# Optimization experiments

Hardware: AMD Instinct MI355X
Metric: run time of the kernel (lower is better)

The kernel has to match this reference:

```python
import jax, jax.numpy as jnp
import numpy as np

B, T, H = 2, 2048, 1024
L = 256          # latent_dim = hidden // compression_ratio
F = 2048         # intermediate_size = hidden * mlp_ratio
E = 7            # routed experts = num_experts - num_shared
K = 2            # top_k
BASE, SCALE_ROPE, EPS = 10000.0, 1.0, 1e-5


def setup_inputs() -> dict:
    key = jax.random.key(0)
    ks = jax.random.split(key, 17)
    s = 0.02
    w = lambda k, shape: jax.random.normal(k, shape, jnp.float32) * s
    return {
        'x': jax.random.normal(ks[0], (B, T, H), jnp.float32),
        'ln1_w': jnp.ones((H,), jnp.float32),
        'ln2_w': jnp.ones((H,), jnp.float32),
        'kv_proj_d': w(ks[1], (L, H)),
        'q_proj_d': w(ks[2], (L, H)),
        'k_proj_u': w(ks[3], (H, L)),
        'q_proj_u': w(ks[4], (H, L)),
        'v_proj_u': w(ks[5], (H, L)),
        'rope_k': w(ks[6], (H, H)),
        'rope_q': w(ks[7], (H, L)),
        'o_proj': w(ks[8], (H, H)),
        'router_w': w(ks[9], (E, H)),
        'routing_bias': jnp.zeros((E,), jnp.float32),
        'sh_gate': w(ks[10], (F, H)),
        'sh_up': w(ks[11], (F, H)),
        'sh_down': w(ks[12], (H, F)),
        'ex_gate': w(ks[13], (E, F, H)),
        'ex_up': w(ks[14], (E, F, H)),
        'ex_down': w(ks[15], (E, H, F)),
    }


def _layernorm(x, w):
    mu = jnp.mean(x, -1, keepdims=True)
    var = jnp.mean(jnp.square(x - mu), -1, keepdims=True)
    return (x - mu) * jax.lax.rsqrt(var + EPS) * w


def _rotate_half(x):
    x1, x2 = jnp.split(x, 2, axis=-1)
    return jnp.concatenate([-x2, x1], axis=-1)


def _rope_cos_sin(seq_len):
    inv_freq = 1.0 / (BASE ** (jnp.arange(0, H, 2, dtype=jnp.float32) / H))
    t = jnp.arange(seq_len, dtype=jnp.float32)
    freqs = jnp.einsum('i,j->ij', t, inv_freq)          # [T, H/2]
    emb = jnp.concatenate([freqs, freqs], axis=-1)      # [T, H]
    return jnp.cos(emb) * SCALE_ROPE, jnp.sin(emb) * SCALE_ROPE


def reference(x, ln1_w, ln2_w, kv_proj_d, q_proj_d, k_proj_u, q_proj_u,
              v_proj_u, rope_k, rope_q, o_proj, router_w, routing_bias,
              sh_gate, sh_up, sh_down, ex_gate, ex_up, ex_down):
    # ---- Multi-head latent attention (num_heads = 1, head_dim = H) ----
    h = _layernorm(x, ln1_w)
    kv_lat = h @ kv_proj_d.T                             # [B,T,L]
    q_lat = h @ q_proj_d.T                               # [B,T,L]
    v = kv_lat @ v_proj_u.T                              # [B,T,H]
    # q,k from q_proj_u/k_proj_u are overwritten by rotary output in the
    # original code; only the rope projections matter.
    q_r = q_lat @ rope_q.T                               # [B,T,H]
    k_r = h @ rope_k.T                                   # [B,T,H]
    cos, sin = _rope_cos_sin(T)
    q = q_r * cos + _rotate_half(q_r) * sin
    k = k_r * cos + _rotate_half(k_r) * sin
    scale = 1.0 / jnp.sqrt(jnp.float32(H))
    scores = jnp.einsum('bqd,bkd->bqk', q, k) * scale    # [B,T,T]
    causal = jnp.tril(jnp.ones((T, T), bool))
    scores = jnp.where(causal, scores, jnp.finfo(scores.dtype).min)
    attn = jax.nn.softmax(scores, axis=-1)
    y = jnp.einsum('bqk,bkd->bqd', attn, v)              # [B,T,H]
    x = x + y @ o_proj.T

    # ---- DeepSeekMoE ----
    h2 = _layernorm(x, ln2_w)
    shared = (jax.nn.silu(h2 @ sh_gate.T) * (h2 @ sh_up.T)) @ sh_down.T
    probs = jax.nn.sigmoid(h2 @ router_w.T + routing_bias)   # [B,T,E]
    top_scores, top_idx = jax.lax.top_k(probs, K)             # [B,T,K]
    # combine[b,t,e] = sum_k top_scores[b,t,k] * (top_idx[b,t,k]==e)
    combine = jnp.sum(top_scores[..., None] *
                      jax.nn.one_hot(top_idx, E, dtype=h2.dtype), axis=-2)
    out = jnp.zeros_like(h2)
    for e in range(E):  # fixed small structural loop over experts
        ye = (jax.nn.silu(h2 @ ex_gate[e].T) * (h2 @ ex_up[e].T)) @ ex_down[e].T
        out = out + combine[..., e:e + 1] * ye
    return x + shared + out
```

## Files before the change

kernel.cpp:

```cpp
#include <hip/hip_runtime.h>
#include <math.h>

#define DEVI static __device__ __forceinline__
typedef __bf16 bf16x8 __attribute__((ext_vector_type(8)));
typedef float  f32x4v __attribute__((ext_vector_type(4)));
typedef unsigned short u16;

DEVI float b2f(u16 u){ union{unsigned int i; float f;} v; v.i=((unsigned int)u)<<16; return v.f; }
DEVI u16 f2b(float f){ union{float f; unsigned int i;} v; v.f=f;
                       unsigned int r=v.i+0x7FFFu+((v.i>>16)&1u); return (u16)(r>>16); }

#define SLOTCAP 9216

__global__ __launch_bounds__(256) void cvt_f32_bf16(const float* __restrict__ s,
                                                    u16* __restrict__ d, int n){
  int i = (blockIdx.x*256 + threadIdx.x)*4;
  if (i < n){
    float4 v = *(const float4*)(s+i);
    ushort4 o; o.x=f2b(v.x); o.y=f2b(v.y); o.z=f2b(v.z); o.w=f2b(v.w);
    *(ushort4*)(d+i) = o;
  }
}

__global__ __launch_bounds__(256) void ln_kernel(const float* __restrict__ x,
                                                 const float* __restrict__ w,
                                                 u16* __restrict__ ob){
  const int row = blockIdx.x, tid = threadIdx.x;
  const float* xr = x + (size_t)row*1024;
  float4 v = *(const float4*)(xr + tid*4);
  float s = v.x+v.y+v.z+v.w;
  for(int m=32;m;m>>=1) s += __shfl_xor(s,m);
  __shared__ float r0[4], r1[4];
  const int wid = tid>>6, lane = tid&63;
  if(!lane) r0[wid]=s;
  __syncthreads();
  const float mean = (r0[0]+r0[1]+r0[2]+r0[3])*(1.f/1024.f);
  float d0=v.x-mean,d1=v.y-mean,d2=v.z-mean,d3=v.w-mean;
  float s2 = d0*d0+d1*d1+d2*d2+d3*d3;
  for(int m=32;m;m>>=1) s2 += __shfl_xor(s2,m);
  if(!lane) r1[wid]=s2;
  __syncthreads();
  const float inv = rsqrtf((r1[0]+r1[1]+r1[2]+r1[3])*(1.f/1024.f) + 1e-5f);
  float4 wv = *(const float4*)(w + tid*4);
  ushort4 o; o.x=f2b(d0*inv*wv.x); o.y=f2b(d1*inv*wv.y);
  o.z=f2b(d2*inv*wv.z); o.w=f2b(d3*inv*wv.w);
  *(ushort4*)(ob + (size_t)row*1024 + tid*4) = o;
}

__global__ __launch_bounds__(256) void rope_kernel(u16* __restrict__ q, u16* __restrict__ k){
  const int row = blockIdx.x;
  const int t = row & 2047;
  u16* qr = q + (size_t)row*1024;
  u16* kr = k + (size_t)row*1024;
  for (int dd = threadIdx.x; dd < 512; dd += 256){
    const float freq = exp2f(-(float)dd * (13.287712379549449f/512.0f));
    const float ang = (float)t * freq;
    float sn, cs; sincosf(ang, &sn, &cs);
    float a = b2f(qr[dd]), b = b2f(qr[dd+512]);
    qr[dd]     = f2b(a*cs - b*sn);
    qr[dd+512] = f2b(b*cs + a*sn);
    float ka = b2f(kr[dd]), kb = b2f(kr[dd+512]);
    kr[dd]     = f2b(ka*cs - kb*sn);
    kr[dd+512] = f2b(kb*cs + ka*sn);
  }
}

__global__ __launch_bounds__(256) void softmax_kernel(const float* __restrict__ S,
                                                      u16* __restrict__ P){
  const int t = blockIdx.x, b = blockIdx.y, tid = threadIdx.x;
  const float* srow = S + ((size_t)b*2048 + t)*2048;
  u16* prow = P + ((size_t)b*2048 + t)*2048;
  const float scale = 0.03125f;
  float e[8]; float mx = -INFINITY;
#pragma unroll
  for(int i=0;i<8;i++){
    int c = tid + i*256;
    float v = (c<=t) ? srow[c]*scale : -INFINITY;
    e[i]=v; mx = fmaxf(mx, v);
  }
  for(int m=32;m;m>>=1) mx = fmaxf(mx, __shfl_xor(mx,m));
  __shared__ float r0[4], r1[4];
  const int wid=tid>>6, lane=tid&63;
  if(!lane) r0[wid]=mx;
  __syncthreads();
  mx = fmaxf(fmaxf(r0[0],r0[1]), fmaxf(r0[2],r0[3]));
  float s=0.f;
#pragma unroll
  for(int i=0;i<8;i++){ float v = (e[i]==-INFINITY)?0.f:__expf(e[i]-mx); e[i]=v; s+=v; }
  for(int m=32;m;m>>=1) s += __shfl_xor(s,m);
  if(!lane) r1[wid]=s;
  __syncthreads();
  const float inv = 1.f/(r1[0]+r1[1]+r1[2]+r1[3]);
#pragma unroll
  for(int i=0;i<8;i++) prow[tid+i*256] = f2b(e[i]*inv);
}

__global__ __launch_bounds__(64) void router_kernel(const float* __restrict__ x1,
    const float* __restrict__ w, const float* __restrict__ rw,
    const float* __restrict__ bias,
    int* __restrict__ te, float* __restrict__ tw, int* __restrict__ cnt){
  const int t = blockIdx.x, lane = threadIdx.x;
  const float* xr = x1 + (size_t)t*1024;
  float xv[16]; float s=0.f;
#pragma unroll
  for(int i=0;i<16;i++){ xv[i] = xr[lane + i*64]; s += xv[i]; }
  for(int m=32;m;m>>=1) s += __shfl_xor(s,m);
  const float mean = s*(1.f/1024.f);
  float s2=0.f;
#pragma unroll
  for(int i=0;i<16;i++){ float d=xv[i]-mean; s2 += d*d; }
  for(int m=32;m;m>>=1) s2 += __shfl_xor(s2,m);
  const float inv = rsqrtf(s2*(1.f/1024.f)+1e-5f);
  float acc[7]={0,0,0,0,0,0,0};
#pragma unroll
  for(int i=0;i<16;i++){
    const int idx = lane + i*64;
    const float hn = (xv[i]-mean)*inv*w[idx];
#pragma unroll
    for(int e=0;e<7;e++) acc[e] += hn * rw[e*1024+idx];
  }
#pragma unroll
  for(int e=0;e<7;e++)
    for(int m=32;m;m>>=1) acc[e] += __shfl_xor(acc[e],m);
  if(lane==0){
    float p[7];
#pragma unroll
    for(int e=0;e<7;e++) p[e] = 1.f/(1.f+expf(-(acc[e]+bias[e])));
    int i1=0;
#pragma unroll
    for(int e=1;e<7;e++) if(p[e]>p[i1]) i1=e;
    int i2=(i1==0)?1:0;
#pragma unroll
    for(int e=0;e<7;e++) if(e!=i1 && p[e]>p[i2]) i2=e;
    te[t*2]=i1; te[t*2+1]=i2; tw[t*2]=p[i1]; tw[t*2+1]=p[i2];
    atomicAdd(&cnt[i1],1); atomicAdd(&cnt[i2],1);
  }
}

__global__ void zero_kernel(int* __restrict__ cnt, int* __restrict__ fill){
  int t = threadIdx.x; if (t<7){ cnt[t]=0; fill[t]=0; }
}

__global__ __launch_bounds__(256) void prep_kernel(const int* __restrict__ cnt,
    int* __restrict__ base, int* __restrict__ ntot,
    int* __restrict__ stok, float* __restrict__ sw, int* __restrict__ eblk){
  __shared__ int sb[8];
  const int tid = threadIdx.x;
  if (tid==0){
    int o=0;
    for(int e=0;e<7;e++){ sb[e]=o; base[e]=o; o += (cnt[e]+127)&~127; }
    sb[7]=o; *ntot=o;
  }
  __syncthreads();
  for(int e=0;e<7;e++){
    const int s = sb[e]+cnt[e], en = sb[e+1];
    for(int i=s+tid; i<en; i+=256){ stok[i]=0; sw[i]=0.f; }
  }
  for(int b=tid; b<SLOTCAP/128; b+=256){
    const int rowst = b*128; int e=6;
#pragma unroll
    for(int q=0;q<7;q++) if (rowst < sb[q+1]){ e=q; break; }
    eblk[b]=e;
  }
}

__global__ __launch_bounds__(256) void scatter_kernel(const int* __restrict__ te,
    const float* __restrict__ tw, const int* __restrict__ base,
    int* __restrict__ fill, int* __restrict__ stok, float* __restrict__ sw){
  const int t = blockIdx.x*256 + threadIdx.x;
  if (t >= 4096) return;
#pragma unroll
  for(int k=0;k<2;k++){
    const int e = te[t*2+k];
    const int s = base[e] + atomicAdd(&fill[e],1);
    stok[s] = t; sw[s] = tw[t*2+k];
  }
}

template<int EPI>
__global__ __launch_bounds__(256,2) void gemm_bt(
    const u16* __restrict__ A, const u16* __restrict__ Bw,
    int K,
    float* __restrict__ Cf, u16* __restrict__ Cb,
    const float* __restrict__ aux,
    const int* __restrict__ gidx, const int* __restrict__ stok,
    const float* __restrict__ sw, const int* __restrict__ ntot,
    const int* __restrict__ eblk, size_t wstride,
    float sc, int ldc)
{
  const int m0 = blockIdx.y*128, n0 = blockIdx.x*128;
  if (ntot && m0 >= *ntot) return;

  __shared__ u16 lA[128*64];
  __shared__ u16 lB[128*64];
  const int tid = threadIdx.x;
  const int wid = tid>>6, lane = tid&63;
  const int wm = wid>>1, wn = wid&1;
  const int lr = lane&15, lk = lane>>4;

  f32x4v acc[4][4];
#pragma unroll
  for(int i=0;i<4;i++)
#pragma unroll
    for(int j=0;j<4;j++) acc[i][j] = (f32x4v){0.f,0.f,0.f,0.f};

  const int selem = tid*8;
  const int srow  = tid>>3;
  const int scol  = (tid&7)*8;
  const u16* Bbase = eblk ? (Bw + (size_t)eblk[blockIdx.y]*wstride) : Bw;
  const u16* Ap[4]; const u16* Bp[4];
#pragma unroll
  for(int is=0;is<4;is++){
    const int ar = m0 + srow + is*32;
    const int arow = gidx ? gidx[ar] : ar;
    Ap[is] = A + (size_t)arow*K + scol;
    Bp[is] = Bbase + (size_t)(n0+srow+is*32)*K + scol;
  }

  for(int k0=0;k0<K;k0+=64){
#pragma unroll
    for(int is=0;is<4;is++){
      __builtin_amdgcn_global_load_lds(
        (const __attribute__((address_space(1))) void*)(Ap[is] + k0),
        (__attribute__((address_space(3))) void*)(&lA[is*2048 + selem]), 16, 0, 0);
      __builtin_amdgcn_global_load_lds(
        (const __attribute__((address_space(1))) void*)(Bp[is] + k0),
        (__attribute__((address_space(3))) void*)(&lB[is*2048 + selem]), 16, 0, 0);
    }
    __syncthreads();
#pragma unroll
    for(int kk=0;kk<64;kk+=32){
      bf16x8 av[4], bv[4];
#pragma unroll
      for(int i=0;i<4;i++) av[i] = *(bf16x8*)&lA[(wm*64+i*16+lr)*64 + kk + lk*8];
#pragma unroll
      for(int j=0;j<4;j++) bv[j] = *(bf16x8*)&lB[(wn*64+j*16+lr)*64 + kk + lk*8];
#pragma unroll
      for(int i=0;i<4;i++)
#pragma unroll
        for(int j=0;j<4;j++)
          acc[i][j] = __builtin_amdgcn_mfma_f32_16x16x32_bf16(av[i], bv[j], acc[i][j], 0,0,0);
    }
    __syncthreads();
  }

#pragma unroll
  for(int i=0;i<4;i++){
    const int rb = m0 + wm*64 + i*16 + lk*4;
#pragma unroll
    for(int j=0;j<4;j++){
      const int col = n0 + wn*64 + j*16 + lr;
      if (EPI==5){
        const int bb = rb>>11, trow = rb&2047;
        ushort4 o;
        o.x=f2b(acc[i][j][0]); o.y=f2b(acc[i][j][1]);
        o.z=f2b(acc[i][j][2]); o.w=f2b(acc[i][j][3]);
        *(ushort4*)(Cb + ((size_t)((bb<<10)+col))*2048 + trow) = o;
      } else {
#pragma unroll
        for(int r=0;r<4;r++){
          const int row = rb + r;
          const size_t idx = (size_t)row*ldc + col;
          const float v = acc[i][j][r];
          if (EPI==0) Cf[idx] = v*sc;
          else if (EPI==1) Cb[idx] = f2b(v);
          else if (EPI==2) Cf[idx] = aux[idx] + v;
          else if (EPI==6){
            const float w = sw[row];
            if (w != 0.f) atomicAdd(&Cf[(size_t)stok[row]*1024 + col], w*v);
          }
          else if (EPI==7){
            const u16* ab = (const u16*)aux;
            const float sg = v/(1.f+expf(-v));
            Cb[idx] = f2b(sg * b2f(ab[idx]));
          }
        }
      }
    }
  }
}

static void run_gemm(int epi, const u16* A, const u16* B, int M,int N,int K,
                     float* Cf, u16* Cb, const float* aux,
                     const int* gidx, const int* stok, const float* sw,
                     const int* ntot, const int* eblk, size_t wstride,
                     float sc, int ldc, hipStream_t st){
  dim3 g((unsigned)(N/128),(unsigned)(M/128)), blk(256);
  switch(epi){
    case 0: gemm_bt<0><<<g,blk,0,st>>>(A,B,K,Cf,Cb,aux,gidx,stok,sw,ntot,eblk,wstride,sc,ldc); break;
    case 1: gemm_bt<1><<<g,blk,0,st>>>(A,B,K,Cf,Cb,aux,gidx,stok,sw,ntot,eblk,wstride,sc,ldc); break;
    case 2: gemm_bt<2><<<g,blk,0,st>>>(A,B,K,Cf,Cb,aux,gidx,stok,sw,ntot,eblk,wstride,sc,ldc); break;
    case 5: gemm_bt<5><<<g,blk,0,st>>>(A,B,K,Cf,Cb,aux,gidx,stok,sw,ntot,eblk,wstride,sc,ldc); break;
    case 6: gemm_bt<6><<<g,blk,0,st>>>(A,B,K,Cf,Cb,aux,gidx,stok,sw,ntot,eblk,wstride,sc,ldc); break;
    case 7: gemm_bt<7><<<g,blk,0,st>>>(A,B,K,Cf,Cb,aux,gidx,stok,sw,ntot,eblk,wstride,sc,ldc); break;
  }
}

extern "C" void kernel_launch(void* const* d_in, const int* in_sizes, int n_in,
                              void* d_out, int out_size, void* d_ws, size_t ws_size,
                              hipStream_t stream){
  (void)in_sizes; (void)n_in; (void)out_size;
  const float* x      = (const float*)d_in[0];
  const float* ln1w   = (const float*)d_in[1];
  const float* ln2w   = (const float*)d_in[2];
  const float* kvd    = (const float*)d_in[3];
  const float* qd     = (const float*)d_in[4];
  const float* vu     = (const float*)d_in[7];
  const float* ropek  = (const float*)d_in[8];
  const float* ropeq  = (const float*)d_in[9];
  const float* oproj  = (const float*)d_in[10];
  const float* routerw= (const float*)d_in[11];
  const float* rbias  = (const float*)d_in[12];
  const float* shg    = (const float*)d_in[13];
  const float* shu    = (const float*)d_in[14];
  const float* shd    = (const float*)d_in[15];
  const float* exg    = (const float*)d_in[16];
  const float* exu    = (const float*)d_in[17];
  const float* exd    = (const float*)d_in[18];
  float* out = (float*)d_out;

  char* wsp = (char*)d_ws; size_t off = 0;
  auto alloc = [&](size_t bytes)->void*{ void* p = wsp+off; off += (bytes+255)&~(size_t)255; return p; };
  u16* wb_kvd = (u16*)alloc((size_t)262144*2);
  u16* wb_qd  = (u16*)alloc((size_t)262144*2);
  u16* wb_vu  = (u16*)alloc((size_t)262144*2);
  u16* wb_rk  = (u16*)alloc((size_t)1048576*2);
  u16* wb_rq  = (u16*)alloc((size_t)262144*2);
  u16* wb_o   = (u16*)alloc((size_t)1048576*2);
  u16* wb_shg = (u16*)alloc((size_t)2097152*2);
  u16* wb_shu = (u16*)alloc((size_t)2097152*2);
  u16* wb_shd = (u16*)alloc((size_t)2097152*2);
  u16* wb_exg = (u16*)alloc((size_t)14680064*2);
  u16* wb_exu = (u16*)alloc((size_t)14680064*2);
  u16* wb_exd = (u16*)alloc((size_t)14680064*2);
  u16* h_b  = (u16*)alloc((size_t)4194304*2);
  u16* kvl  = (u16*)alloc((size_t)1048576*2);
  u16* ql   = (u16*)alloc((size_t)1048576*2);
  u16* vT   = (u16*)alloc((size_t)4194304*2);
  u16* q_ro = (u16*)alloc((size_t)4194304*2);
  u16* k_ro = (u16*)alloc((size_t)4194304*2);
  u16* y_b  = (u16*)alloc((size_t)4194304*2);
  float* x1 = (float*)alloc((size_t)4194304*4);
  u16* h2_b = (u16*)alloc((size_t)4194304*2);
  char* U   = (char*)alloc((size_t)50331648);
  float* gS = (float*)U;
  u16*   aP = (u16*)(U + 33554432);
  u16*  act = (u16*)U;
  int*   te   = (int*)alloc(8192*4);
  float* tw   = (float*)alloc(8192*4);
  int*   cnt  = (int*)alloc(64);
  int*   base = (int*)alloc(64);
  int*   fill = (int*)alloc(64);
  int*   ntot = (int*)alloc(64);
  int*   stok = (int*)alloc(SLOTCAP*4);
  float* sw   = (float*)alloc(SLOTCAP*4);
  int*   eblk = (int*)alloc((SLOTCAP/128)*4);
  if (off > ws_size) return;

  auto cvt = [&](const float* s, u16* d, int n){
    cvt_f32_bf16<<<dim3((unsigned)(n/1024)),dim3(256),0,stream>>>(s,d,n);
  };
  cvt(kvd, wb_kvd, 262144);  cvt(qd, wb_qd, 262144);   cvt(vu, wb_vu, 262144);
  cvt(ropek, wb_rk, 1048576); cvt(ropeq, wb_rq, 262144); cvt(oproj, wb_o, 1048576);
  cvt(shg, wb_shg, 2097152); cvt(shu, wb_shu, 2097152); cvt(shd, wb_shd, 2097152);
  cvt(exg, wb_exg, 14680064); cvt(exu, wb_exu, 14680064); cvt(exd, wb_exd, 14680064);

  const size_t WST = 2097152;

  ln_kernel<<<dim3(4096),dim3(256),0,stream>>>(x, ln1w, h_b);
  run_gemm(1, h_b, wb_kvd, 4096, 256,1024, 0,kvl,0, 0,0,0,0,0,0, 1.f, 256, stream);
  run_gemm(1, h_b, wb_qd,  4096, 256,1024, 0,ql, 0, 0,0,0,0,0,0, 1.f, 256, stream);
  run_gemm(5, kvl, wb_vu,  4096,1024, 256, 0,vT, 0, 0,0,0,0,0,0, 1.f, 0,   stream);
  run_gemm(1, ql,  wb_rq,  4096,1024, 256, 0,q_ro,0,0,0,0,0,0,0, 1.f, 1024,stream);
  run_gemm(1, h_b, wb_rk,  4096,1024,1024, 0,k_ro,0,0,0,0,0,0,0, 1.f, 1024,stream);
  rope_kernel<<<dim3(4096),dim3(256),0,stream>>>(q_ro, k_ro);
  for(int b=0;b<2;b++)
    run_gemm(0, q_ro+(size_t)b*2097152, k_ro+(size_t)b*2097152, 2048,2048,1024,
             gS+(size_t)b*4194304, 0, 0, 0,0,0,0,0,0, 1.f, 2048, stream);
  softmax_kernel<<<dim3(2048,2),dim3(256),0,stream>>>(gS, aP);
  for(int b=0;b<2;b++)
    run_gemm(1, aP+(size_t)b*4194304, vT+(size_t)b*2097152, 2048,1024,2048,
             0, y_b+(size_t)b*2097152, 0, 0,0,0,0,0,0, 1.f, 1024, stream);
  run_gemm(2, y_b, wb_o, 4096,1024,1024, x1, 0, x, 0,0,0,0,0,0, 1.f, 1024, stream);

  ln_kernel<<<dim3(4096),dim3(256),0,stream>>>(x1, ln2w, h2_b);
  zero_kernel<<<dim3(1),dim3(64),0,stream>>>(cnt, fill);
  router_kernel<<<dim3(4096),dim3(64),0,stream>>>(x1, ln2w, routerw, rbias, te, tw, cnt);
  prep_kernel<<<dim3(1),dim3(256),0,stream>>>(cnt, base, ntot, stok, sw, eblk);
  scatter_kernel<<<dim3(16),dim3(256),0,stream>>>(te, tw, base, fill, stok, sw);

  run_gemm(1, h2_b, wb_shu, 4096,2048,1024, 0, aP, 0, 0,0,0,0,0,0, 1.f, 2048, stream);
  run_gemm(7, h2_b, wb_shg, 4096,2048,1024, 0, aP, (const float*)aP, 0,0,0,0,0,0, 1.f, 2048, stream);
  run_gemm(2, aP,   wb_shd, 4096,1024,2048, out, 0, x1, 0,0,0,0,0,0, 1.f, 1024, stream);

  run_gemm(1, h2_b, wb_exu, SLOTCAP,2048,1024, 0, act, 0,
           stok, 0,0, ntot, eblk, WST, 1.f, 2048, stream);
  run_gemm(7, h2_b, wb_exg, SLOTCAP,2048,1024, 0, act, (const float*)act,
           stok, 0,0, ntot, eblk, WST, 1.f, 2048, stream);
  run_gemm(6, act, wb_exd, SLOTCAP,1024,2048, out, 0, 0,
           0, stok, sw, ntot, eblk, WST, 1.f, 1024, stream);
}
```

Measured before the change: 1.057 ms.

## Add 256x256 double-buffered 8-wave GEMM with causal skip and batched launches

Introduces a new 512-thread GEMM kernel with 256x256 tiles, double-buffered swizzled LDS, staged asynchronous loads interleaved with MFMA phases, and s_setprio. The large GEMMs, including the MoE expert GEMMs, move to it. The score GEMM skips tiles above the causal diagonal, and the per-batch GEMMs now run as one launch using a z dimension. The router is vectorised with four tokens per block, global atomics are replaced by shared-memory histogram and scatter kernels, and expert slot padding grows to 256 rows. The larger tiles raise data reuse and cut launch count, at the cost of more padding waste in the expert GEMMs and higher register and LDS pressure.

```diff
diff --git a/kernel.cpp b/kernel.cpp
--- a/kernel.cpp
+++ b/kernel.cpp
@@ -10,7 +10,7 @@
 DEVI u16 f2b(float f){ union{float f; unsigned int i;} v; v.f=f;
                        unsigned int r=v.i+0x7FFFu+((v.i>>16)&1u); return (u16)(r>>16); }
 
-#define SLOTCAP 9216
+#define SLOTCAP 10240
 
 __global__ __launch_bounds__(256) void cvt_f32_bf16(const float* __restrict__ s,
                                                     u16* __restrict__ d, int n){
@@ -95,29 +95,44 @@
   for(int i=0;i<8;i++) prow[tid+i*256] = f2b(e[i]*inv);
 }
 
-__global__ __launch_bounds__(64) void router_kernel(const float* __restrict__ x1,
+__global__ __launch_bounds__(256) void router_kernel(const float* __restrict__ x1,
     const float* __restrict__ w, const float* __restrict__ rw,
     const float* __restrict__ bias,
-    int* __restrict__ te, float* __restrict__ tw, int* __restrict__ cnt){
-  const int t = blockIdx.x, lane = threadIdx.x;
+    int* __restrict__ te, float* __restrict__ tw){
+  const int t = blockIdx.x*4 + (threadIdx.x>>6);
+  const int lane = threadIdx.x&63;
   const float* xr = x1 + (size_t)t*1024;
-  float xv[16]; float s=0.f;
-#pragma unroll
-  for(int i=0;i<16;i++){ xv[i] = xr[lane + i*64]; s += xv[i]; }
+  float4 xv[4]; float s=0.f;
+#pragma unroll
+  for(int i=0;i<4;i++){ xv[i] = *(const float4*)(xr + i*256 + lane*4);
+                        s += xv[i].x+xv[i].y+xv[i].z+xv[i].w; }
   for(int m=32;m;m>>=1) s += __shfl_xor(s,m);
   const float mean = s*(1.f/1024.f);
   float s2=0.f;
 #pragma unroll
-  for(int i=0;i<16;i++){ float d=xv[i]-mean; s2 += d*d; }
+  for(int i=0;i<4;i++){
+    float a=xv[i].x-mean,b=xv[i].y-mean,c=xv[i].z-mean,d=xv[i].w-mean;
+    s2 += a*a+b*b+c*c+d*d;
+  }
   for(int m=32;m;m>>=1) s2 += __shfl_xor(s2,m);
   const float inv = rsqrtf(s2*(1.f/1024.f)+1e-5f);
-  float acc[7]={0,0,0,0,0,0,0};
-#pragma unroll
-  for(int i=0;i<16;i++){
-    const int idx = lane + i*64;
-    const float hn = (xv[i]-mean)*inv*w[idx];
-#pragma unroll
-    for(int e=0;e<7;e++) acc[e] += hn * rw[e*1024+idx];
+  float hn[16];
+#pragma unroll
+  for(int i=0;i<4;i++){
+    const float4 wv = *(const float4*)(w + i*256 + lane*4);
+    hn[i*4+0]=(xv[i].x-mean)*inv*wv.x; hn[i*4+1]=(xv[i].y-mean)*inv*wv.y;
+    hn[i*4+2]=(xv[i].z-mean)*inv*wv.z; hn[i*4+3]=(xv[i].w-mean)*inv*wv.w;
+  }
+  float acc[7];
+#pragma unroll
+  for(int e=0;e<7;e++){
+    float a=0.f;
+#pragma unroll
+    for(int i=0;i<4;i++){
+      const float4 rv = *(const float4*)(rw + (size_t)e*1024 + i*256 + lane*4);
+      a += hn[i*4+0]*rv.x + hn[i*4+1]*rv.y + hn[i*4+2]*rv.z + hn[i*4+3]*rv.w;
+    }
+    acc[e]=a;
   }
 #pragma unroll
   for(int e=0;e<7;e++)
@@ -133,12 +148,18 @@
 #pragma unroll
     for(int e=0;e<7;e++) if(e!=i1 && p[e]>p[i2]) i2=e;
     te[t*2]=i1; te[t*2+1]=i2; tw[t*2]=p[i1]; tw[t*2+1]=p[i2];
-    atomicAdd(&cnt[i1],1); atomicAdd(&cnt[i2],1);
-  }
-}
-
-__global__ void zero_kernel(int* __restrict__ cnt, int* __restrict__ fill){
-  int t = threadIdx.x; if (t<7){ cnt[t]=0; fill[t]=0; }
+  }
+}
+
+__global__ __launch_bounds__(256) void hist_kernel(const int* __restrict__ te,
+                                                   int* __restrict__ cnt){
+  __shared__ int h[7];
+  const int tid = threadIdx.x;
+  if (tid<7) h[tid]=0;
+  __syncthreads();
+  for(int i=tid;i<8192;i+=256) atomicAdd(&h[te[i]],1);
+  __syncthreads();
+  if (tid<7) cnt[tid]=h[tid];
 }
 
 __global__ __launch_bounds__(256) void prep_kernel(const int* __restrict__ cnt,
@@ -148,7 +169,7 @@
   const int tid = threadIdx.x;
   if (tid==0){
     int o=0;
-    for(int e=0;e<7;e++){ sb[e]=o; base[e]=o; o += (cnt[e]+127)&~127; }
+    for(int e=0;e<7;e++){ sb[e]=o; base[e]=o; o += (cnt[e]+255)&~255; }
     sb[7]=o; *ntot=o;
   }
   __syncthreads();
@@ -156,44 +177,225 @@
     const int s = sb[e]+cnt[e], en = sb[e+1];
     for(int i=s+tid; i<en; i+=256){ stok[i]=0; sw[i]=0.f; }
   }
-  for(int b=tid; b<SLOTCAP/128; b+=256){
-    const int rowst = b*128; int e=6;
+  for(int b=tid; b<SLOTCAP/256; b+=256){
+    const int rowst = b*256; int e=6;
 #pragma unroll
     for(int q=0;q<7;q++) if (rowst < sb[q+1]){ e=q; break; }
     eblk[b]=e;
   }
 }
 
-__global__ __launch_bounds__(256) void scatter_kernel(const int* __restrict__ te,
+__global__ __launch_bounds__(1024) void scatter_kernel(const int* __restrict__ te,
     const float* __restrict__ tw, const int* __restrict__ base,
-    int* __restrict__ fill, int* __restrict__ stok, float* __restrict__ sw){
-  const int t = blockIdx.x*256 + threadIdx.x;
-  if (t >= 4096) return;
-#pragma unroll
-  for(int k=0;k<2;k++){
-    const int e = te[t*2+k];
-    const int s = base[e] + atomicAdd(&fill[e],1);
-    stok[s] = t; sw[s] = tw[t*2+k];
-  }
-}
+    int* __restrict__ stok, float* __restrict__ sw){
+  __shared__ int lf[7];
+  const int tid = threadIdx.x;
+  if (tid<7) lf[tid]=0;
+  __syncthreads();
+  for(int t=tid; t<4096; t+=1024){
+#pragma unroll
+    for(int k=0;k<2;k++){
+      const int e = te[t*2+k];
+      const int s = base[e] + atomicAdd(&lf[e],1);
+      stok[s] = t; sw[s] = tw[t*2+k];
+    }
+  }
+}
+
+#define BAR8 asm volatile("s_barrier" ::: "memory")
+
+#define PHASE_Q(LAB, Q, DOSTAGE) { \
+  bf16x8 av[2][2]; \
+  _Pragma("unroll") for(int m2=0;m2<2;m2++) \
+    _Pragma("unroll") for(int ks=0;ks<2;ks++) \
+      av[m2][ks] = *(const bf16x8*)((LAB) + aoff[(Q)*2+m2][ks]); \
+  DOSTAGE; \
+  __builtin_amdgcn_s_setprio(1); \
+  _Pragma("unroll") for(int ks=0;ks<2;ks++) \
+    _Pragma("unroll") for(int m2=0;m2<2;m2++) \
+      _Pragma("unroll") for(int nf=0;nf<4;nf++) \
+        acc[(Q)*2+m2][nf] = __builtin_amdgcn_mfma_f32_16x16x32_bf16( \
+            av[m2][ks], bv[nf][ks], acc[(Q)*2+m2][nf],0,0,0); \
+  __builtin_amdgcn_s_setprio(0); }
+
+#define READ_B(LBB) { \
+  _Pragma("unroll") for(int nf=0;nf<4;nf++) \
+    _Pragma("unroll") for(int ks=0;ks<2;ks++) \
+      bv[nf][ks] = *(const bf16x8*)((LBB) + boff[nf][ks]); }
 
 template<int EPI>
-__global__ __launch_bounds__(256,2) void gemm_bt(
-    const u16* __restrict__ A, const u16* __restrict__ Bw,
-    int K,
-    float* __restrict__ Cf, u16* __restrict__ Cb,
-    const float* __restrict__ aux,
+__global__ __launch_bounds__(512,2) void gemm8(
+    const u16* __restrict__ A, const u16* __restrict__ Bw, int K, int causal,
+    float* __restrict__ Cf, u16* __restrict__ Cb, const float* __restrict__ aux,
     const int* __restrict__ gidx, const int* __restrict__ stok,
     const float* __restrict__ sw, const int* __restrict__ ntot,
     const int* __restrict__ eblk, size_t wstride,
-    float sc, int ldc)
+    int ldc, size_t zsa, size_t zsb, size_t zsc)
 {
-  const int m0 = blockIdx.y*128, n0 = blockIdx.x*128;
+  const int m0 = blockIdx.y*256, n0 = blockIdx.x*256;
   if (ntot && m0 >= *ntot) return;
-
+  if (causal && n0 > m0 + 255) return;
+  const int z = blockIdx.z;
+  const u16* Ag = A + (size_t)z*zsa;
+  const u16* Bg = Bw + (size_t)z*zsb + (eblk ? (size_t)eblk[blockIdx.y]*wstride : 0);
+
+  __shared__ u16 lA[2][16384];
+  __shared__ u16 lB[2][16384];
+
+  const int tid = threadIdx.x;
+  const int wid = tid>>6, lane = tid&63;
+  const int wm = wid>>2, wn = wid&3;
+  const int lr = lane&15, lk = lane>>4;
+
+  const int srow = tid>>3;
+  const int ssw  = ((tid&7)*16) ^ ((srow&7)<<4);
+  const u16* Asrc[4]; const u16* Bsrc[4];
+#pragma unroll
+  for(int is=0; is<4; is++){
+    const int ar = m0 + is*64 + srow;
+    const int garow = gidx ? gidx[ar] : ar;
+    Asrc[is] = Ag + (size_t)garow*K + (ssw>>1);
+    Bsrc[is] = Bg + (size_t)(n0 + is*64 + srow)*K + (ssw>>1);
+  }
+  const int ldsoff = tid*16;
+
+  auto SB4 = [&](int kt){
+    const int c = kt&1; const int kb = kt*64;
+#pragma unroll
+    for(int is=0; is<4; is++)
+      __builtin_amdgcn_global_load_lds(
+        (const __attribute__((address_space(1))) void*)(Bsrc[is] + kb),
+        (__attribute__((address_space(3))) void*)((char*)&lB[c][0] + is*8192 + ldsoff), 16,0,0);
+  };
+  auto SA2 = [&](int kt, int p){
+    const int c = kt&1; const int kb = kt*64;
+#pragma unroll
+    for(int ii=0; ii<2; ii++){
+      const int is = p + ii*2;
+      __builtin_amdgcn_global_load_lds(
+        (const __attribute__((address_space(1))) void*)(Asrc[is] + kb),
+        (__attribute__((address_space(3))) void*)((char*)&lA[c][0] + is*8192 + ldsoff), 16,0,0);
+    }
+  };
+
+  int aoff[8][2], boff[4][2];
+#pragma unroll
+  for(int mf=0; mf<8; mf++){
+    const int r = wm*128 + mf*16 + lr;
+#pragma unroll
+    for(int ks=0; ks<2; ks++){
+      const int cb = ks*64 + lk*16;
+      aoff[mf][ks] = r*128 + (cb ^ ((r&7)<<4));
+    }
+  }
+#pragma unroll
+  for(int nf=0; nf<4; nf++){
+    const int r = wn*64 + nf*16 + lr;
+#pragma unroll
+    for(int ks=0; ks<2; ks++){
+      const int cb = ks*64 + lk*16;
+      boff[nf][ks] = r*128 + (cb ^ ((r&7)<<4));
+    }
+  }
+
+  f32x4v acc[8][4];
+#pragma unroll
+  for(int i=0;i<8;i++)
+#pragma unroll
+    for(int j=0;j<4;j++) acc[i][j] = (f32x4v){0.f,0.f,0.f,0.f};
+  bf16x8 bv[4][2];
+
+  const char* lab0 = (const char*)&lA[0][0]; const char* lab1 = (const char*)&lA[1][0];
+  const char* lbb0 = (const char*)&lB[0][0]; const char* lbb1 = (const char*)&lB[1][0];
+
+  const int nt = K>>6;
+  SB4(0); SA2(0,0); SA2(0,1);
+  SB4(1); SA2(1,0);
+
+  for(int t=0; t<nt; t+=2){
+    const bool s2 = (t+2)<nt, s3 = (t+3)<nt;
+    SA2(t+1,1);
+    asm volatile("s_waitcnt vmcnt(8)" ::: "memory");
+    BAR8;
+    READ_B(lbb0);
+    PHASE_Q(lab0, 0, ;);
+    BAR8;
+    PHASE_Q(lab0, 1, if(s2) SB4(t+2););
+    BAR8;
+    PHASE_Q(lab0, 2, if(s2) SA2(t+2,0););
+    BAR8;
+    PHASE_Q(lab0, 3, ;);
+    BAR8;
+    if(s2) SA2(t+2,1);
+    if(s2) { asm volatile("s_waitcnt vmcnt(8)" ::: "memory"); }
+    else   { asm volatile("s_waitcnt vmcnt(0)" ::: "memory"); }
+    BAR8;
+    READ_B(lbb1);
+    PHASE_Q(lab1, 0, ;);
+    BAR8;
+    PHASE_Q(lab1, 1, if(s3) SB4(t+3););
+    BAR8;
+    PHASE_Q(lab1, 2, if(s3) SA2(t+3,0););
+    BAR8;
+    PHASE_Q(lab1, 3, ;);
+    BAR8;
+  }
+
+  float* CfZ = Cf ? Cf + (size_t)z*zsc : (float*)0;
+  u16*   CbZ = Cb ? Cb + (size_t)z*zsc : (u16*)0;
+#pragma unroll
+  for(int mf=0; mf<8; mf++){
+    const int rb = m0 + wm*128 + mf*16 + lk*4;
+#pragma unroll
+    for(int nf=0; nf<4; nf++){
+      const int col = n0 + wn*64 + nf*16 + lr;
+#pragma unroll
+      for(int r=0; r<4; r++){
+        const int row = rb + r;
+        const size_t idx = (size_t)row*ldc + col;
+        const float v = acc[mf][nf][r];
+        if (EPI==0) CfZ[idx] = v;
+        else if (EPI==1) CbZ[idx] = f2b(v);
+        else if (EPI==2) CfZ[idx] = aux[idx] + v;
+        else if (EPI==6){
+          const float w2 = sw[row];
+          if (w2 != 0.f) atomicAdd(&Cf[(size_t)stok[row]*1024 + col], w2*v);
+        }
+        else if (EPI==7){
+          const u16* ab = (const u16*)aux;
+          const float sg = v/(1.f+expf(-v));
+          CbZ[idx] = f2b(sg * b2f(ab[idx]));
+        }
+      }
+    }
+  }
+}
+
+static void run_gemm8(int epi, const u16* A, const u16* B, int Mblk, int N, int K,
+                      float* Cf, u16* Cb, const float* aux,
+                      const int* gidx, const int* stok, const float* sw,
+                      const int* ntot, const int* eblk, size_t wstride,
+                      int ldc, int Z, size_t zsa, size_t zsb, size_t zsc,
+                      int causal, hipStream_t st){
+  dim3 g((unsigned)(N/256),(unsigned)Mblk,(unsigned)Z), blk(512);
+  switch(epi){
+    case 0: gemm8<0><<<g,blk,0,st>>>(A,B,K,causal,Cf,Cb,aux,gidx,stok,sw,ntot,eblk,wstride,ldc,zsa,zsb,zsc); break;
+    case 1: gemm8<1><<<g,blk,0,st>>>(A,B,K,causal,Cf,Cb,aux,gidx,stok,sw,ntot,eblk,wstride,ldc,zsa,zsb,zsc); break;
+    case 2: gemm8<2><<<g,blk,0,st>>>(A,B,K,causal,Cf,Cb,aux,gidx,stok,sw,ntot,eblk,wstride,ldc,zsa,zsb,zsc); break;
+    case 6: gemm8<6><<<g,blk,0,st>>>(A,B,K,causal,Cf,Cb,aux,gidx,stok,sw,ntot,eblk,wstride,ldc,zsa,zsb,zsc); break;
+    case 7: gemm8<7><<<g,blk,0,st>>>(A,B,K,causal,Cf,Cb,aux,gidx,stok,sw,ntot,eblk,wstride,ldc,zsa,zsb,zsc); break;
+  }
+}
+
+template<int EPI>
+__global__ __launch_bounds__(256,2) void gemm_bt(
+    const u16* __restrict__ A, const u16* __restrict__ Bw, int K,
+    u16* __restrict__ Cb, int ldc)
+{
   __shared__ u16 lA[128*64];
   __shared__ u16 lB[128*64];
   const int tid = threadIdx.x;
+  const int m0 = blockIdx.y*128, n0 = blockIdx.x*128;
   const int wid = tid>>6, lane = tid&63;
   const int wm = wid>>1, wn = wid&1;
   const int lr = lane&15, lk = lane>>4;
@@ -207,24 +409,17 @@
   const int selem = tid*8;
   const int srow  = tid>>3;
   const int scol  = (tid&7)*8;
-  const u16* Bbase = eblk ? (Bw + (size_t)eblk[blockIdx.y]*wstride) : Bw;
-  const u16* Ap[4]; const u16* Bp[4];
-#pragma unroll
-  for(int is=0;is<4;is++){
-    const int ar = m0 + srow + is*32;
-    const int arow = gidx ? gidx[ar] : ar;
-    Ap[is] = A + (size_t)arow*K + scol;
-    Bp[is] = Bbase + (size_t)(n0+srow+is*32)*K + scol;
-  }
+  const u16* Ab = A  + (size_t)(m0+srow)*K + scol;
+  const u16* Bb = Bw + (size_t)(n0+srow)*K + scol;
 
   for(int k0=0;k0<K;k0+=64){
 #pragma unroll
     for(int is=0;is<4;is++){
       __builtin_amdgcn_global_load_lds(
-        (const __attribute__((address_space(1))) void*)(Ap[is] + k0),
+        (const __attribute__((address_space(1))) void*)(Ab + k0 + (size_t)is*32*K),
         (__attribute__((address_space(3))) void*)(&lA[is*2048 + selem]), 16, 0, 0);
       __builtin_amdgcn_global_load_lds(
-        (const __attribute__((address_space(1))) void*)(Bp[is] + k0),
+        (const __attribute__((address_space(1))) void*)(Bb + k0 + (size_t)is*32*K),
         (__attribute__((address_space(3))) void*)(&lB[is*2048 + selem]), 16, 0, 0);
     }
     __syncthreads();
@@ -258,41 +453,9 @@
         *(ushort4*)(Cb + ((size_t)((bb<<10)+col))*2048 + trow) = o;
       } else {
 #pragma unroll
-        for(int r=0;r<4;r++){
-          const int row = rb + r;
-          const size_t idx = (size_t)row*ldc + col;
-          const float v = acc[i][j][r];
-          if (EPI==0) Cf[idx] = v*sc;
-          else if (EPI==1) Cb[idx] = f2b(v);
-          else if (EPI==2) Cf[idx] = aux[idx] + v;
-          else if (EPI==6){
-            const float w = sw[row];
-            if (w != 0.f) atomicAdd(&Cf[(size_t)stok[row]*1024 + col], w*v);
-          }
-          else if (EPI==7){
-            const u16* ab = (const u16*)aux;
-            const float sg = v/(1.f+expf(-v));
-            Cb[idx] = f2b(sg * b2f(ab[idx]));
-          }
-        }
+        for(int r=0;r<4;r++) Cb[(size_t)(rb+r)*ldc + col] = f2b(acc[i][j][r]);
       }
     }
-  }
-}
-
-static void run_gemm(int epi, const u16* A, const u16* B, int M,int N,int K,
-                     float* Cf, u16* Cb, const float* aux,
-                     const int* gidx, const int* stok, const float* sw,
-                     const int* ntot, const int* eblk, size_t wstride,
-                     float sc, int ldc, hipStream_t st){
-  dim3 g((unsigned)(N/128),(unsigned)(M/128)), blk(256);
-  switch(epi){
-    case 0: gemm_bt<0><<<g,blk,0,st>>>(A,B,K,Cf,Cb,aux,gidx,stok,sw,ntot,eblk,wstride,sc,ldc); break;
-    case 1: gemm_bt<1><<<g,blk,0,st>>>(A,B,K,Cf,Cb,aux,gidx,stok,sw,ntot,eblk,wstride,sc,ldc); break;
-    case 2: gemm_bt<2><<<g,blk,0,st>>>(A,B,K,Cf,Cb,aux,gidx,stok,sw,ntot,eblk,wstride,sc,ldc); break;
-    case 5: gemm_bt<5><<<g,blk,0,st>>>(A,B,K,Cf,Cb,aux,gidx,stok,sw,ntot,eblk,wstride,sc,ldc); break;
-    case 6: gemm_bt<6><<<g,blk,0,st>>>(A,B,K,Cf,Cb,aux,gidx,stok,sw,ntot,eblk,wstride,sc,ldc); break;
-    case 7: gemm_bt<7><<<g,blk,0,st>>>(A,B,K,Cf,Cb,aux,gidx,stok,sw,ntot,eblk,wstride,sc,ldc); break;
   }
 }
 
@@ -342,19 +505,18 @@
   u16* y_b  = (u16*)alloc((size_t)4194304*2);
   float* x1 = (float*)alloc((size_t)4194304*4);
   u16* h2_b = (u16*)alloc((size_t)4194304*2);
-  char* U   = (char*)alloc((size_t)50331648);
-  float* gS = (float*)U;
-  u16*   aP = (u16*)(U + 33554432);
-  u16*  act = (u16*)U;
+  char* U   = (char*)alloc((size_t)58720256);
+  u16*   aP = (u16*)U;
+  float* gS = (float*)(U + 16777216);
+  u16*  act = (u16*)(U + 16777216);
   int*   te   = (int*)alloc(8192*4);
   float* tw   = (float*)alloc(8192*4);
   int*   cnt  = (int*)alloc(64);
   int*   base = (int*)alloc(64);
-  int*   fill = (int*)alloc(64);
   int*   ntot = (int*)alloc(64);
   int*   stok = (int*)alloc(SLOTCAP*4);
   float* sw   = (float*)alloc(SLOTCAP*4);
-  int*   eblk = (int*)alloc((SLOTCAP/128)*4);
+  int*   eblk = (int*)alloc((SLOTCAP/256)*4);
   if (off > ws_size) return;
 
   auto cvt = [&](const float* s, u16* d, int n){
@@ -368,35 +530,33 @@
   const size_t WST = 2097152;
 
   ln_kernel<<<dim3(4096),dim3(256),0,stream>>>(x, ln1w, h_b);
-  run_gemm(1, h_b, wb_kvd, 4096, 256,1024, 0,kvl,0, 0,0,0,0,0,0, 1.f, 256, stream);
-  run_gemm(1, h_b, wb_qd,  4096, 256,1024, 0,ql, 0, 0,0,0,0,0,0, 1.f, 256, stream);
-  run_gemm(5, kvl, wb_vu,  4096,1024, 256, 0,vT, 0, 0,0,0,0,0,0, 1.f, 0,   stream);
-  run_gemm(1, ql,  wb_rq,  4096,1024, 256, 0,q_ro,0,0,0,0,0,0,0, 1.f, 1024,stream);
-  run_gemm(1, h_b, wb_rk,  4096,1024,1024, 0,k_ro,0,0,0,0,0,0,0, 1.f, 1024,stream);
+  gemm_bt<1><<<dim3(2,32),dim3(256),0,stream>>>(h_b, wb_kvd, 1024, kvl, 256);
+  gemm_bt<1><<<dim3(2,32),dim3(256),0,stream>>>(h_b, wb_qd,  1024, ql,  256);
+  gemm_bt<5><<<dim3(8,32),dim3(256),0,stream>>>(kvl, wb_vu,  256,  vT,  0);
+  gemm_bt<1><<<dim3(8,32),dim3(256),0,stream>>>(ql,  wb_rq,  256,  q_ro,1024);
+  run_gemm8(1, h_b, wb_rk, 16,1024,1024, 0,k_ro,0, 0,0,0,0,0,0, 1024, 1,0,0,0, 0, stream);
   rope_kernel<<<dim3(4096),dim3(256),0,stream>>>(q_ro, k_ro);
-  for(int b=0;b<2;b++)
-    run_gemm(0, q_ro+(size_t)b*2097152, k_ro+(size_t)b*2097152, 2048,2048,1024,
-             gS+(size_t)b*4194304, 0, 0, 0,0,0,0,0,0, 1.f, 2048, stream);
+  run_gemm8(0, q_ro, k_ro, 8,2048,1024, gS,0,0, 0,0,0,0,0,0, 2048,
+            2, 2097152,2097152,4194304, 1, stream);
   softmax_kernel<<<dim3(2048,2),dim3(256),0,stream>>>(gS, aP);
-  for(int b=0;b<2;b++)
-    run_gemm(1, aP+(size_t)b*4194304, vT+(size_t)b*2097152, 2048,1024,2048,
-             0, y_b+(size_t)b*2097152, 0, 0,0,0,0,0,0, 1.f, 1024, stream);
-  run_gemm(2, y_b, wb_o, 4096,1024,1024, x1, 0, x, 0,0,0,0,0,0, 1.f, 1024, stream);
+  run_gemm8(1, aP, vT, 8,1024,2048, 0,y_b,0, 0,0,0,0,0,0, 1024,
+            2, 4194304,2097152,2097152, 0, stream);
+  run_gemm8(2, y_b, wb_o, 16,1024,1024, x1,0,x, 0,0,0,0,0,0, 1024, 1,0,0,0, 0, stream);
 
   ln_kernel<<<dim3(4096),dim3(256),0,stream>>>(x1, ln2w, h2_b);
-  zero_kernel<<<dim3(1),dim3(64),0,stream>>>(cnt, fill);
-  router_kernel<<<dim3(4096),dim3(64),0,stream>>>(x1, ln2w, routerw, rbias, te, tw, cnt);
+  router_kernel<<<dim3(1024),dim3(256),0,stream>>>(x1, ln2w, routerw, rbias, te, tw);
+  hist_kernel<<<dim3(1),dim3(256),0,stream>>>(te, cnt);
   prep_kernel<<<dim3(1),dim3(256),0,stream>>>(cnt, base, ntot, stok, sw, eblk);
-  scatter_kernel<<<dim3(16),dim3(256),0,stream>>>(te, tw, base, fill, stok, sw);
-
-  run_gemm(1, h2_b, wb_shu, 4096,2048,1024, 0, aP, 0, 0,0,0,0,0,0, 1.f, 2048, stream);
-  run_gemm(7, h2_b, wb_shg, 4096,2048,1024, 0, aP, (const float*)aP, 0,0,0,0,0,0, 1.f, 2048, stream);
-  run_gemm(2, aP,   wb_shd, 4096,1024,2048, out, 0, x1, 0,0,0,0,0,0, 1.f, 1024, stream);
-
-  run_gemm(1, h2_b, wb_exu, SLOTCAP,2048,1024, 0, act, 0,
-           stok, 0,0, ntot, eblk, WST, 1.f, 2048, stream);
-  run_gemm(7, h2_b, wb_exg, SLOTCAP,2048,1024, 0, act, (const float*)act,
-           stok, 0,0, ntot, eblk, WST, 1.f, 2048, stream);
-  run_gemm(6, act, wb_exd, SLOTCAP,1024,2048, out, 0, 0,
-           0, stok, sw, ntot, eblk, WST, 1.f, 1024, stream);
-}
+  scatter_kernel<<<dim3(1),dim3(1024),0,stream>>>(te, tw, base, stok, sw);
+
+  run_gemm8(1, h2_b, wb_shu, 16,2048,1024, 0,aP,0, 0,0,0,0,0,0, 2048, 1,0,0,0, 0, stream);
+  run_gemm8(7, h2_b, wb_shg, 16,2048,1024, 0,aP,(const float*)aP, 0,0,0,0,0,0, 2048, 1,0,0,0, 0, stream);
+  run_gemm8(2, aP, wb_shd, 16,1024,2048, out,0,x1, 0,0,0,0,0,0, 1024, 1,0,0,0, 0, stream);
+
+  run_gemm8(1, h2_b, wb_exu, SLOTCAP/256,2048,1024, 0,act,0,
+            stok,0,0, ntot, eblk, WST, 2048, 1,0,0,0, 0, stream);
+  run_gemm8(7, h2_b, wb_exg, SLOTCAP/256,2048,1024, 0,act,(const float*)act,
+            stok,0,0, ntot, eblk, WST, 2048, 1,0,0,0, 0, stream);
+  run_gemm8(6, act, wb_exd, SLOTCAP/256,1024,2048, out,0,0,
+            0,stok,sw, ntot, eblk, WST, 1024, 1,0,0,0, 0, stream);
+}
```

After: 953.9 us. 1.11x faster.
